# Kernel optimization log

Hardware: AMD Instinct MI355X
Metric: run time of the kernel (lower is better)

## Reference

```python
import jax, jax.numpy as jnp
import numpy as np

ATOM_DIM = 64
BOND_DIM = 64
B, N_ATOMS, N_BONDS = 32, 256, 512


def setup_inputs() -> dict:
    key = jax.random.key(0)
    k1, k2, k3, k4 = jax.random.split(key, 4)
    atom_state = jax.random.normal(k1, (B, N_ATOMS, ATOM_DIM), dtype=jnp.float32)
    bond_state = jax.random.normal(k2, (B, N_BONDS, BOND_DIM), dtype=jnp.float32)
    connectivity = jax.random.randint(k3, (B, N_BONDS, 2), 0, N_ATOMS, dtype=jnp.int64)
    # glorot-ish scale for the learned bond->matrix projection
    scale = (2.0 / (BOND_DIM + ATOM_DIM * ATOM_DIM)) ** 0.5
    bond_transform = jax.random.normal(k4, (BOND_DIM, ATOM_DIM * ATOM_DIM), dtype=jnp.float32) * scale
    return {
        "atom_state": atom_state,
        "bond_state": bond_state,
        "connectivity": connectivity,
        "bond_transform": bond_transform,
    }


def reference(atom_state, bond_state, connectivity, bond_transform):
    # src atom per edge: gather along atom axis with batch dim (tf.gather batch_dims=1)
    src_idx = connectivity[:, :, 0]                                  # [B, E]
    src_atoms = jnp.take_along_axis(
        atom_state, src_idx[:, :, None], axis=1)                    # [B, E, D]
    # bond embedding -> per-edge DxD matrix
    W = bond_transform.reshape(BOND_DIM, ATOM_DIM, ATOM_DIM)         # [K, D, D]
    bond_weights = jnp.einsum('bek,kij->beij', bond_state, W)        # [B, E, D, D]
    # per-edge matrix-vector message: A_e @ h_src
    messages = jnp.einsum('beij,bej->bei', bond_weights, src_atoms)  # [B, E, D]
    return messages
```

## Files before the change

### kernel.cpp

```cpp
#include <hip/hip_runtime.h>
#include <stdint.h>


#define NATOMS 256
#define DIM 64
#define BT 128

typedef _Float16 f16;
typedef _Float16 f16x2 __attribute__((ext_vector_type(2)));
typedef _Float16 f16x8 __attribute__((ext_vector_type(8)));
typedef float f32x16 __attribute__((ext_vector_type(16)));

union H8 { f16x8 v8; f16x2 v2[4]; };

__global__ __launch_bounds__(256) void prep_w2f(const float* __restrict__ bt,
                                                f16* __restrict__ w2f) {
    const int d  = blockIdx.x * 256 + threadIdx.x;
    const int k  = d >> 9, c = d & 511;
    const int ch = c >> 8, s = (c >> 6) & 3, l = c & 63;
    const int col = ch * 32 + (l & 31);
    const float* src = bt + (size_t)k * 4096 + col * 64 + s * 16 + (l >> 5) * 8;
    const float4 p = *reinterpret_cast<const float4*>(src);
    const float4 q = *reinterpret_cast<const float4*>(src + 4);
    const f16x8 h = { (f16)p.x, (f16)p.y, (f16)p.z, (f16)p.w,
                      (f16)q.x, (f16)q.y, (f16)q.z, (f16)q.w };
    reinterpret_cast<f16x8*>(w2f)[d] = h;
}

static __device__ __forceinline__ unsigned swz16(unsigned lane) {
    return (lane * 16u) ^ ((lane & 0x38u) << 1);
}

__global__ __launch_bounds__(512, 1) void bond_msg(
    const float* __restrict__ atom, const float* __restrict__ bond,
    const int* __restrict__ conn, const f16* __restrict__ w2f,
    float* __restrict__ out)
{
    __shared__ __align__(16) unsigned char smem[65536];

    const int tid  = threadIdx.x;
    const int lane = tid & 63;
    const int w    = tid >> 6;
    const int mt   = w & 3;
    const int kh   = w >> 2;
    const int lo   = lane & 31;
    const int hi   = lane >> 5;
    const int blk  = blockIdx.x;
    const int btile = blk >> 1;
    const int ch   = blk & 1;
    const int bond0 = btile * BT;

    const char* gw = reinterpret_cast<const char*>(w2f)
                   + (size_t)ch * 4096 + (size_t)lane * 16;
    char* lstw = reinterpret_cast<char*>(smem) + kh * 16384 + mt * 4096
               + lane * 16;
    const char* lrd = reinterpret_cast<const char*>(smem) + kh * 16384 + lane * 16;

    const int e = bond0 + mt * 32 + lo;
    const int ia = conn[e * 2];
    f16x2 bp[32];
    {
        const float* brow = bond + (size_t)e * DIM + kh * 32;
        #pragma unroll
        for (int q = 0; q < 8; ++q) {
            const float4 v = *reinterpret_cast<const float4*>(brow + q * 4);
            const f16 a0 = (f16)v.x, a1 = (f16)v.y, a2 = (f16)v.z, a3 = (f16)v.w;
            bp[q*4+0] = (f16x2){a0,a0}; bp[q*4+1] = (f16x2){a1,a1};
            bp[q*4+2] = (f16x2){a2,a2}; bp[q*4+3] = (f16x2){a3,a3};
        }
    }

    const float* arow = atom + (size_t)(btile >> 2) * (NATOMS * DIM)
                      + (size_t)ia * DIM;
    f16x2 srcv[4][4];
    #pragma unroll
    for (int s = 0; s < 4; ++s) {
        const int j0 = s * 16 + hi * 8;
        const float4 p0 = *reinterpret_cast<const float4*>(arow + j0);
        const float4 p1 = *reinterpret_cast<const float4*>(arow + j0 + 4);
        srcv[s][0] = (f16x2){ (f16)p0.x, (f16)p0.y };
        srcv[s][1] = (f16x2){ (f16)p0.z, (f16)p0.w };
        srcv[s][2] = (f16x2){ (f16)p1.x, (f16)p1.y };
        srcv[s][3] = (f16x2){ (f16)p1.z, (f16)p1.w };
    }

    f16x8 sA[4], sB[4];

    #define LOADR(S, p) do { if ((p) < 8) {                               \
        const char* _g = gw + (size_t)(kh * 32 + (p) * 4 + mt) * 8192;    \
        S[0] = *reinterpret_cast<const f16x8*>(_g);                       \
        S[1] = *reinterpret_cast<const f16x8*>(_g + 1024);                \
        S[2] = *reinterpret_cast<const f16x8*>(_g + 2048);                \
        S[3] = *reinterpret_cast<const f16x8*>(_g + 3072);                \
    } } while (0)

    #define WRITE(S, p) do { if ((p) < 8) {                               \
        char* _l = lstw + ((p) & 1) * 32768;                              \
        *reinterpret_cast<f16x8*>(_l)        = S[0];                      \
        *reinterpret_cast<f16x8*>(_l + 1024) = S[1];                      \
        *reinterpret_cast<f16x8*>(_l + 2048) = S[2];                      \
        *reinterpret_cast<f16x8*>(_l + 3072) = S[3];                      \
    } } while (0)

    #define LDSBAR() do {                                                 \
        asm volatile("s_waitcnt lgkmcnt(0)" ::: "memory");                \
        __builtin_amdgcn_s_barrier();                                     \
        __builtin_amdgcn_sched_barrier(0);                                \
    } while (0)

    f32x16 acc = {};

    #define COMPUTE(p) do {                                               \
        const char* _rb = lrd + ((p) & 1) * 32768;                        \
        _Pragma("unroll")                                                 \
        for (int q = 0; q < 4; ++q) {                                     \
            const f16x2 _c = bp[(p) * 4 + q];                             \
            _Pragma("unroll")                                             \
            for (int s = 0; s < 4; ++s) {                                 \
                const f16x8 bf = *reinterpret_cast<const f16x8*>(         \
                    _rb + q * 4096 + s * 1024);                           \
                H8 _a;                                                    \
                _Pragma("unroll")                                         \
                for (int t = 0; t < 4; ++t) _a.v2[t] = _c * srcv[s][t];   \
                acc = __builtin_amdgcn_mfma_f32_32x32x16_f16(_a.v8, bf, acc, 0, 0, 0); \
            }                                                             \
        }                                                                 \
    } while (0)

    #define STEP(p, S) do {                                               \
        LOADR(S, (p) + 1);                                                \
        __builtin_amdgcn_sched_barrier(0);                                \
        COMPUTE(p);                                                       \
        __builtin_amdgcn_sched_barrier(0);                                \
        WRITE(S, (p) + 1);   \
        LDSBAR();                                                         \
    } while (0)

    LOADR(sA, 0);
    WRITE(sA, 0);
    LDSBAR();

    STEP(0, sB); STEP(1, sA); STEP(2, sB); STEP(3, sA);
    STEP(4, sB); STEP(5, sA); STEP(6, sB);
    COMPUTE(7);

    #undef STEP
    #undef COMPUTE
    #undef LDSBAR
    #undef WRITE
    #undef LOADR

    __syncthreads();
    if (kh == 1) {
        const unsigned so = swz16((unsigned)lane);
        #pragma unroll
        for (int g = 0; g < 4; ++g) {
            float4 v = { acc[4*g+0], acc[4*g+1], acc[4*g+2], acc[4*g+3] };
            *reinterpret_cast<float4*>(smem + mt*4096 + g*1024 + so) = v;
        }
    }
    __syncthreads();
    if (kh == 0) {
        const unsigned so = swz16((unsigned)lane);
        #pragma unroll
        for (int g = 0; g < 4; ++g) {
            const float4 v = *reinterpret_cast<const float4*>(
                smem + mt*4096 + g*1024 + so);
            acc[4*g+0] += v.x; acc[4*g+1] += v.y;
            acc[4*g+2] += v.z; acc[4*g+3] += v.w;
        }
        const int colb = ch * 32 + lo;
        #pragma unroll
        for (int r = 0; r < 16; ++r) {
            const int rl = (r & 3) + 8 * (r >> 2) + 4 * hi;
            out[(size_t)(bond0 + mt * 32 + rl) * 64 + colb] = acc[r];
        }
    }
}

__global__ __launch_bounds__(256) void bond_fallback(
    const float* __restrict__ atom, const float* __restrict__ bond,
    const int* __restrict__ conn, const float* __restrict__ bt,
    float* __restrict__ out)
{
    __shared__ float Wk[4096];
    __shared__ float srcs[4][64];
    __shared__ float bnds[4][64];
    const int blk = blockIdx.x;
    const int e0 = blk * 4;
    const int b = e0 >> 9;
    const int t = threadIdx.x;
    const int il = t & 63, eg = t >> 6;
    const int e = e0 + eg;
    const int ia = conn[e * 2];
    srcs[eg][il] = atom[(size_t)b * (NATOMS * DIM) + (size_t)ia * DIM + il];
    bnds[eg][il] = bond[(size_t)e * DIM + il];
    float acc = 0.f;
    for (int k = 0; k < 64; ++k) {
        __syncthreads();
        #pragma unroll
        for (int c = 0; c < 4; ++c) {
            float4 v = reinterpret_cast<const float4*>(bt + (size_t)k * 4096)[t + c * 256];
            reinterpret_cast<float4*>(Wk)[t + c * 256] = v;
        }
        __syncthreads();
        float s = 0.f;
        #pragma unroll
        for (int j = 0; j < 64; ++j) s += Wk[il * 64 + j] * srcs[eg][j];
        acc += bnds[eg][k] * s;
    }
    out[(size_t)e * DIM + il] = acc;
}

extern "C" void kernel_launch(void* const* d_in, const int* in_sizes, int n_in,
                              void* d_out, int out_size, void* d_ws, size_t ws_size,
                              hipStream_t stream) {
    const float* atom = (const float*)d_in[0];
    const float* bond = (const float*)d_in[1];
    const int*   conn = (const int*)d_in[2];
    const float* bt   = (const float*)d_in[3];
    float* out = (float*)d_out;

    if (ws_size >= (size_t)64 * 4096 * sizeof(f16)) {
        f16* w2f = (f16*)d_ws;
        prep_w2f<<<128, 256, 0, stream>>>(bt, w2f);
        bond_msg<<<256, 512, 0, stream>>>(atom, bond, conn, w2f, out);
    } else {
        bond_fallback<<<4096, 256, 0, stream>>>(atom, bond, conn, bt, out);
    }
}
```

Before: 22.00 us.

## Fuse weight fp16 conversion into main kernel, drop prep pass and fallback

Removes the separate prep kernel that converted and re-laid out the bond transform to fp16 in workspace. The main kernel now loads fp32 weights directly from global memory, converts them to fp16 in registers, and writes them to the swizzled LDS layout through per-lane offsets. This saves a kernel launch and a global round trip, but doubles the global bytes read per block and adds conversion work inside the pipelined loop. The no-workspace fallback path is deleted.

Result: slower. 30.06 us (+36.6%).

```diff
diff --git a/kernel.cpp b/kernel.cpp
--- a/kernel.cpp
+++ b/kernel.cpp
@@ -12,20 +12,7 @@
 typedef float f32x16 __attribute__((ext_vector_type(16)));
 
 union H8 { f16x8 v8; f16x2 v2[4]; };
-
-__global__ __launch_bounds__(256) void prep_w2f(const float* __restrict__ bt,
-                                                f16* __restrict__ w2f) {
-    const int d  = blockIdx.x * 256 + threadIdx.x;
-    const int k  = d >> 9, c = d & 511;
-    const int ch = c >> 8, s = (c >> 6) & 3, l = c & 63;
-    const int col = ch * 32 + (l & 31);
-    const float* src = bt + (size_t)k * 4096 + col * 64 + s * 16 + (l >> 5) * 8;
-    const float4 p = *reinterpret_cast<const float4*>(src);
-    const float4 q = *reinterpret_cast<const float4*>(src + 4);
-    const f16x8 h = { (f16)p.x, (f16)p.y, (f16)p.z, (f16)p.w,
-                      (f16)q.x, (f16)q.y, (f16)q.z, (f16)q.w };
-    reinterpret_cast<f16x8*>(w2f)[d] = h;
-}
+union F8 { float4 v4[2]; float f[8]; };
 
 static __device__ __forceinline__ unsigned swz16(unsigned lane) {
     return (lane * 16u) ^ ((lane & 0x38u) << 1);
@@ -33,7 +20,7 @@
 
 __global__ __launch_bounds__(512, 1) void bond_msg(
     const float* __restrict__ atom, const float* __restrict__ bond,
-    const int* __restrict__ conn, const f16* __restrict__ w2f,
+    const int* __restrict__ conn, const float* __restrict__ bt,
     float* __restrict__ out)
 {
     __shared__ __align__(16) unsigned char smem[65536];
@@ -50,10 +37,15 @@
     const int ch   = blk & 1;
     const int bond0 = btile * BT;
 
-    const char* gw = reinterpret_cast<const char*>(w2f)
-                   + (size_t)ch * 4096 + (size_t)lane * 16;
-    char* lstw = reinterpret_cast<char*>(smem) + kh * 16384 + mt * 4096
-               + lane * 16;
+    const float* gsrc = bt + (size_t)ch * 2048 + (size_t)lane * 32;
+    char* lbase = reinterpret_cast<char*>(smem) + kh * 16384 + mt * 4096;
+    unsigned woff[4];
+    #pragma unroll
+    for (int c = 0; c < 4; ++c) {
+        const int s    = 2 * (lane & 1) + (c >> 1);
+        const int slot = (c & 1) * 32 + (lane >> 1);
+        woff[c] = (unsigned)(s * 1024 + slot * 16);
+    }
     const char* lrd = reinterpret_cast<const char*>(smem) + kh * 16384 + lane * 16;
 
     const int e = bond0 + mt * 32 + lo;
@@ -84,22 +76,27 @@
         srcv[s][3] = (f16x2){ (f16)p1.z, (f16)p1.w };
     }
 
-    f16x8 sA[4], sB[4];
+    F8 sA[4], sB[4];
 
     #define LOADR(S, p) do { if ((p) < 8) {                               \
-        const char* _g = gw + (size_t)(kh * 32 + (p) * 4 + mt) * 8192;    \
-        S[0] = *reinterpret_cast<const f16x8*>(_g);                       \
-        S[1] = *reinterpret_cast<const f16x8*>(_g + 1024);                \
-        S[2] = *reinterpret_cast<const f16x8*>(_g + 2048);                \
-        S[3] = *reinterpret_cast<const f16x8*>(_g + 3072);                \
+        const float* _g = gsrc + (size_t)(kh * 32 + (p) * 4 + mt) * 4096; \
+        _Pragma("unroll")                                                 \
+        for (int c = 0; c < 4; ++c) {                                     \
+            S[c].v4[0] = *reinterpret_cast<const float4*>(_g + c * 8);    \
+            S[c].v4[1] = *reinterpret_cast<const float4*>(_g + c * 8 + 4);\
+        }                                                                 \
     } } while (0)
 
     #define WRITE(S, p) do { if ((p) < 8) {                               \
-        char* _l = lstw + ((p) & 1) * 32768;                              \
-        *reinterpret_cast<f16x8*>(_l)        = S[0];                      \
-        *reinterpret_cast<f16x8*>(_l + 1024) = S[1];                      \
-        *reinterpret_cast<f16x8*>(_l + 2048) = S[2];                      \
-        *reinterpret_cast<f16x8*>(_l + 3072) = S[3];                      \
+        char* _l = lbase + ((p) & 1) * 32768;                             \
+        _Pragma("unroll")                                                 \
+        for (int c = 0; c < 4; ++c) {                                     \
+            const f16x8 h = { (f16)S[c].f[0], (f16)S[c].f[1],             \
+                              (f16)S[c].f[2], (f16)S[c].f[3],             \
+                              (f16)S[c].f[4], (f16)S[c].f[5],             \
+                              (f16)S[c].f[6], (f16)S[c].f[7] };           \
+            *reinterpret_cast<f16x8*>(_l + woff[c]) = h;                  \
+        }                                                                 \
     } } while (0)
 
     #define LDSBAR() do {                                                 \
@@ -132,7 +129,7 @@
         __builtin_amdgcn_sched_barrier(0);                                \
         COMPUTE(p);                                                       \
         __builtin_amdgcn_sched_barrier(0);                                \
-        WRITE(S, (p) + 1);   \
+        WRITE(S, (p) + 1);    \
         LDSBAR();                                                         \
     } while (0)
 
@@ -178,40 +175,6 @@
     }
 }
 
-__global__ __launch_bounds__(256) void bond_fallback(
-    const float* __restrict__ atom, const float* __restrict__ bond,
-    const int* __restrict__ conn, const float* __restrict__ bt,
-    float* __restrict__ out)
-{
-    __shared__ float Wk[4096];
-    __shared__ float srcs[4][64];
-    __shared__ float bnds[4][64];
-    const int blk = blockIdx.x;
-    const int e0 = blk * 4;
-    const int b = e0 >> 9;
-    const int t = threadIdx.x;
-    const int il = t & 63, eg = t >> 6;
-    const int e = e0 + eg;
-    const int ia = conn[e * 2];
-    srcs[eg][il] = atom[(size_t)b * (NATOMS * DIM) + (size_t)ia * DIM + il];
-    bnds[eg][il] = bond[(size_t)e * DIM + il];
-    float acc = 0.f;
-    for (int k = 0; k < 64; ++k) {
-        __syncthreads();
-        #pragma unroll
-        for (int c = 0; c < 4; ++c) {
-            float4 v = reinterpret_cast<const float4*>(bt + (size_t)k * 4096)[t + c * 256];
-            reinterpret_cast<float4*>(Wk)[t + c * 256] = v;
-        }
-        __syncthreads();
-        float s = 0.f;
-        #pragma unroll
-        for (int j = 0; j < 64; ++j) s += Wk[il * 64 + j] * srcs[eg][j];
-        acc += bnds[eg][k] * s;
-    }
-    out[(size_t)e * DIM + il] = acc;
-}
-
 extern "C" void kernel_launch(void* const* d_in, const int* in_sizes, int n_in,
                               void* d_out, int out_size, void* d_ws, size_t ws_size,
                               hipStream_t stream) {
@@ -221,11 +184,5 @@
     const float* bt   = (const float*)d_in[3];
     float* out = (float*)d_out;
 
-    if (ws_size >= (size_t)64 * 4096 * sizeof(f16)) {
-        f16* w2f = (f16*)d_ws;
-        prep_w2f<<<128, 256, 0, stream>>>(bt, w2f);
-        bond_msg<<<256, 512, 0, stream>>>(atom, bond, conn, w2f, out);
-    } else {
-        bond_fallback<<<4096, 256, 0, stream>>>(atom, bond, conn, bt, out);
-    }
+    bond_msg<<<256, 512, 0, stream>>>(atom, bond, conn, bt, out);
 }
```
